# Optimization experiments

Measured on AMD Instinct MI355X. Metric: run time of the kernel, lower is better.

The kernel has to match this reference:

```python
import jax, jax.numpy as jnp
import numpy as np

BATCH = 262144
N_ASSETS = 64
N_GROUPS = 8
ITERS = 20
EPS = 1e-9


def setup_inputs() -> dict:
    key = jax.random.key(0)
    kx = jax.random.fold_in(key, 1)
    x = jax.random.uniform(kx, (BATCH, N_ASSETS), dtype=jnp.float32)
    x = x / jnp.sum(x, axis=-1, keepdims=True)  # roughly simplex-like raw weights
    box_lb = jnp.zeros((N_ASSETS,), jnp.float32)          # port_type[0] = 0 (long-only)
    box_ub = jnp.full((N_ASSETS,), 0.3, jnp.float32)      # per-asset cap from _build_constraints
    # one-hot group membership matrix: asset i belongs to group i % N_GROUPS
    gid = np.arange(N_ASSETS) % N_GROUPS
    A = np.zeros((N_GROUPS, N_ASSETS), np.float32)
    A[gid, np.arange(N_ASSETS)] = 1.0
    group_A = jnp.asarray(A)
    group_lb = jnp.full((N_GROUPS,), 0.05, jnp.float32)
    group_ub = jnp.full((N_GROUPS,), 0.5, jnp.float32)
    return {"x": x, "box_lb": box_lb, "box_ub": box_ub, "group_A": group_A,
            "group_lb": group_lb, "group_ub": group_ub, "num_iterations": ITERS}


def _dykstra(x, box_lb, box_ub, group_A, group_lb, group_ub, num_iterations):
    n = x.shape[-1]
    norm_sq = jnp.sum(group_A * group_A, axis=-1)  # (G,)

    def box_simplex(w):
        w = jnp.clip(w, box_lb, box_ub)
        return w - (jnp.sum(w, axis=-1, keepdims=True) - 1.0) / n

    def group_step(w, g):
        a, lb, ub, ns = g  # a: (N,), scalars lb/ub/ns
        Aw = w @ a  # (B,)
        w = jnp.where((Aw > ub)[:, None], w - ((Aw - ub) / (ns + EPS))[:, None] * a, w)
        Aw = w @ a  # recomputed on updated w, matching the TF layer
        w = jnp.where((Aw < lb)[:, None], w - ((Aw - lb) / (ns + EPS))[:, None] * a, w)
        return w, None

    def body(i, w):
        w = box_simplex(w)
        w, _ = jax.lax.scan(group_step, w, (group_A, group_lb, group_ub, norm_sq))
        return w

    w = jax.lax.fori_loop(0, num_iterations, body, x)
    return box_simplex(w)


def reference(x, box_lb, box_ub, group_A, group_lb, group_ub, num_iterations):
    return _dykstra(x, box_lb, box_ub, group_A, group_lb, group_ub, num_iterations)
```

## Files before the change

kernel.cpp:

```cpp
#include <hip/hip_runtime.h>


#define NA 64
#define NG 8
#define TOL 1e-6f

__device__ __forceinline__ float row8_allreduce_sum(float v) {
    int j = __builtin_amdgcn_update_dpp(0, __builtin_bit_cast(int, v),
                                        0xB1 , 0xF, 0xF, true);
    v += __builtin_bit_cast(float, j);
    j = __builtin_amdgcn_update_dpp(0, __builtin_bit_cast(int, v),
                                    0x4E , 0xF, 0xF, true);
    v += __builtin_bit_cast(float, j);
    j = __builtin_amdgcn_ds_swizzle(__builtin_bit_cast(int, v), 0x101F );
    v += __builtin_bit_cast(float, j);
    return v;
}

__device__ __forceinline__ bool structural_ok(const float* __restrict__ box_lb,
                                              const float* __restrict__ box_ub,
                                              const float* __restrict__ group_A,
                                              int l) {
    const float lb0 = box_lb[0], ub0 = box_ub[0];
    bool ok = (box_lb[l] == lb0) && (box_ub[l] == ub0) && (lb0 <= ub0);
#pragma unroll
    for (int g = 0; g < NG; ++g) {
        const float expect = ((l & 7) == g) ? 1.0f : 0.0f;
        ok = ok && (group_A[g * NA + l] == expect);
    }
    return __all(ok);
}

__global__ __launch_bounds__(256) void proj_fast(
    const float* __restrict__ x,
    const float* __restrict__ box_lb,
    const float* __restrict__ box_ub,
    const float* __restrict__ group_A,
    const float* __restrict__ group_lb,
    const float* __restrict__ group_ub,
    const int*  __restrict__ num_iter,
    float* __restrict__ out,
    int nrows)
{
    if (!structural_ok(box_lb, box_ub, group_A, threadIdx.x & 63)) return;

    const int t = blockIdx.x * blockDim.x + threadIdx.x;
    const int r = t >> 3;
    const int c = t & 7;
    if (r >= nrows) return;

    const float* __restrict__ xr = x + (size_t)r * NA;
    float* __restrict__ outr = out + (size_t)r * NA;

    float w[8];
#pragma unroll
    for (int k = 0; k < 8; ++k) w[k] = xr[k * 8 + c];

    const float lb0 = box_lb[0], ub0 = box_ub[0];
    const float glb = group_lb[c];
    const float gub = group_ub[c];

    const int iters = *num_iter;

    const float inv8 = 1.0f / (8.0f + 1e-9f);

    for (int it = 0; it < iters; ++it) {
#pragma unroll
        for (int k = 0; k < 8; ++k)
            w[k] = __builtin_amdgcn_fmed3f(w[k], lb0, ub0);
        const float s01 = w[0] + w[1], s23 = w[2] + w[3];
        const float s45 = w[4] + w[5], s67 = w[6] + w[7];
        const float dota = (s01 + s23) + (s45 + s67);

        const float S = row8_allreduce_sum(dota);
        const float shift = fmaf(S, 1.0f / NA, -1.0f / NA);

        const float Aw  = fmaf(-8.0f, shift, dota);
        const float e1  = fmaxf(Aw - gub, 0.0f);
        const float Aw2 = Aw - e1;
        const float e2  = fminf(Aw2 - glb, 0.0f);
        const float d   = (e1 + e2) * inv8;
        const float u   = shift + d;

#pragma unroll
        for (int k = 0; k < 8; ++k) w[k] -= u;

        if (__all(__builtin_fabsf(shift) < TOL && __builtin_fabsf(d) < TOL))
            break;
    }

#pragma unroll
    for (int k = 0; k < 8; ++k)
        w[k] = __builtin_amdgcn_fmed3f(w[k], lb0, ub0);
    const float s01 = w[0] + w[1], s23 = w[2] + w[3];
    const float s45 = w[4] + w[5], s67 = w[6] + w[7];
    const float S = row8_allreduce_sum((s01 + s23) + (s45 + s67));
    const float shift = fmaf(S, 1.0f / NA, -1.0f / NA);

#pragma unroll
    for (int k = 0; k < 8; ++k)
        outr[k * 8 + c] = w[k] - shift;
}

__global__ __launch_bounds__(256) void proj_generic(
    const float* __restrict__ x,
    const float* __restrict__ box_lb,
    const float* __restrict__ box_ub,
    const float* __restrict__ group_A,
    const float* __restrict__ group_lb,
    const float* __restrict__ group_ub,
    const int*  __restrict__ num_iter,
    float* __restrict__ out,
    int nrows)
{
    if (structural_ok(box_lb, box_ub, group_A, threadIdx.x & 63)) return;

    const int r = blockIdx.x * blockDim.x + threadIdx.x;
    if (r >= nrows) return;

    const float* __restrict__ xr = x + (size_t)r * NA;
    float* __restrict__ outr = out + (size_t)r * NA;

    float w[NA];
#pragma unroll
    for (int j = 0; j < NA; ++j) w[j] = xr[j];

    const int iters = *num_iter;

    for (int it = 0; it < iters; ++it) {
        float S = 0.0f;
#pragma unroll
        for (int j = 0; j < NA; ++j) {
            w[j] = fminf(fmaxf(w[j], box_lb[j]), box_ub[j]);
            S += w[j];
        }
        const float shift = (S - 1.0f) * (1.0f / NA);
#pragma unroll
        for (int j = 0; j < NA; ++j) w[j] -= shift;

        for (int g = 0; g < NG; ++g) {
            const float* __restrict__ a = group_A + g * NA;
            float ns = 0.0f, Aw = 0.0f;
#pragma unroll
            for (int j = 0; j < NA; ++j) {
                const float av = a[j];
                ns = fmaf(av, av, ns);
                Aw = fmaf(av, w[j], Aw);
            }
            const float invg = 1.0f / (ns + 1e-9f);
            const float gub = group_ub[g], glb = group_lb[g];
            const float d1 = (Aw > gub) ? (Aw - gub) * invg : 0.0f;
#pragma unroll
            for (int j = 0; j < NA; ++j) w[j] = fmaf(-d1, a[j], w[j]);
            float Aw2 = 0.0f;
#pragma unroll
            for (int j = 0; j < NA; ++j) Aw2 = fmaf(a[j], w[j], Aw2);
            const float d2 = (Aw2 < glb) ? (Aw2 - glb) * invg : 0.0f;
#pragma unroll
            for (int j = 0; j < NA; ++j) w[j] = fmaf(-d2, a[j], w[j]);
        }
    }
    float S = 0.0f;
#pragma unroll
    for (int j = 0; j < NA; ++j) {
        w[j] = fminf(fmaxf(w[j], box_lb[j]), box_ub[j]);
        S += w[j];
    }
    const float shift = (S - 1.0f) * (1.0f / NA);
#pragma unroll
    for (int j = 0; j < NA; ++j) outr[j] = w[j] - shift;
}

extern "C" void kernel_launch(void* const* d_in, const int* in_sizes, int n_in,
                              void* d_out, int out_size, void* d_ws, size_t ws_size,
                              hipStream_t stream) {
    const float* x        = (const float*)d_in[0];
    const float* box_lb   = (const float*)d_in[1];
    const float* box_ub   = (const float*)d_in[2];
    const float* group_A  = (const float*)d_in[3];
    const float* group_lb = (const float*)d_in[4];
    const float* group_ub = (const float*)d_in[5];
    const int*   num_iter = (const int*)d_in[6];
    float* out = (float*)d_out;

    const int nrows = in_sizes[0] / NA;

    {
        const int total = nrows * 8;
        const int block = 256;
        const int grid = (total + block - 1) / block;
        proj_fast<<<grid, block, 0, stream>>>(x, box_lb, box_ub, group_A,
                                              group_lb, group_ub, num_iter,
                                              out, nrows);
    }
    {
        const int block = 256;
        const int grid = (nrows + block - 1) / block;
        proj_generic<<<grid, block, 0, stream>>>(x, box_lb, box_ub, group_A,
                                                 group_lb, group_ub, num_iter,
                                                 out, nrows);
    }
}
```

Before: 135.3 us.

## Merge fast and generic kernels and stage row I/O through LDS with float4

Combines the structured fast path and the generic fallback into one kernel that picks the path per wave at runtime, which removes the second kernel launch. Row loads and stores now go through shared memory as contiguous float4 accesses and are then redistributed to the 8-lanes-per-row layout. The generic path is also rewritten to use 8 lanes per row with DPP reductions. The cost is added LDS traffic and two block barriers.

```diff
diff --git a/kernel.cpp b/kernel.cpp
--- a/kernel.cpp
+++ b/kernel.cpp
@@ -4,6 +4,9 @@
 #define NA 64
 #define NG 8
 #define TOL 1e-6f
+#define RS 72
+#define ROWS_PER_BLOCK 32
+#define ROWS_PER_WAVE 8
 
 __device__ __forceinline__ float row8_allreduce_sum(float v) {
     int j = __builtin_amdgcn_update_dpp(0, __builtin_bit_cast(int, v),
@@ -17,21 +20,7 @@
     return v;
 }
 
-__device__ __forceinline__ bool structural_ok(const float* __restrict__ box_lb,
-                                              const float* __restrict__ box_ub,
-                                              const float* __restrict__ group_A,
-                                              int l) {
-    const float lb0 = box_lb[0], ub0 = box_ub[0];
-    bool ok = (box_lb[l] == lb0) && (box_ub[l] == ub0) && (lb0 <= ub0);
-#pragma unroll
-    for (int g = 0; g < NG; ++g) {
-        const float expect = ((l & 7) == g) ? 1.0f : 0.0f;
-        ok = ok && (group_A[g * NA + l] == expect);
-    }
-    return __all(ok);
-}
-
-__global__ __launch_bounds__(256) void proj_fast(
+__global__ __launch_bounds__(256) void proj_kernel(
     const float* __restrict__ x,
     const float* __restrict__ box_lb,
     const float* __restrict__ box_ub,
@@ -42,133 +31,161 @@
     float* __restrict__ out,
     int nrows)
 {
-    if (!structural_ok(box_lb, box_ub, group_A, threadIdx.x & 63)) return;
-
-    const int t = blockIdx.x * blockDim.x + threadIdx.x;
-    const int r = t >> 3;
-    const int c = t & 7;
-    if (r >= nrows) return;
-
-    const float* __restrict__ xr = x + (size_t)r * NA;
-    float* __restrict__ outr = out + (size_t)r * NA;
-
+    __shared__ float lds[ROWS_PER_BLOCK * RS];
+
+    const int tid  = threadIdx.x;
+    const int wave = tid >> 6;
+    const int lane = tid & 63;
+    const int lr   = lane >> 3;
+    const int c    = lane & 7;
+
+    const size_t wrow0 = (size_t)blockIdx.x * ROWS_PER_BLOCK + (size_t)wave * ROWS_PER_WAVE;
+    const size_t r = wrow0 + (size_t)lr;
+    const bool fullwave = (wrow0 + ROWS_PER_WAVE) <= (size_t)nrows;
+    const bool valid = r < (size_t)nrows;
+
+    float* lw = lds + wave * ROWS_PER_WAVE * RS;
+
+    float4 v0, v1;
+    if (fullwave) {
+        const float4* src = reinterpret_cast<const float4*>(x + wrow0 * NA);
+        v0 = src[lane];
+        v1 = src[lane + 64];
+    }
+
+    const float lb0 = box_lb[0], ub0 = box_ub[0];
+    bool ok = (box_lb[lane] == lb0) && (box_ub[lane] == ub0) && (lb0 <= ub0);
+#pragma unroll
+    for (int g = 0; g < NG; ++g) {
+        const float expect = ((lane & 7) == g) ? 1.0f : 0.0f;
+        ok = ok && (group_A[g * NA + lane] == expect);
+    }
+    const bool fast = __all(ok);
+
+    if (fullwave) {
+        *reinterpret_cast<float4*>(lw + (lane >> 4) * RS + (lane & 15) * 4) = v0;
+        *reinterpret_cast<float4*>(lw + ((lane >> 4) + 4) * RS + (lane & 15) * 4) = v1;
+    }
+    __syncthreads();
     float w[8];
-#pragma unroll
-    for (int k = 0; k < 8; ++k) w[k] = xr[k * 8 + c];
-
-    const float lb0 = box_lb[0], ub0 = box_ub[0];
-    const float glb = group_lb[c];
-    const float gub = group_ub[c];
+    if (fullwave) {
+#pragma unroll
+        for (int k = 0; k < 8; ++k) w[k] = lw[lr * RS + k * 8 + c];
+    } else if (valid) {
+#pragma unroll
+        for (int k = 0; k < 8; ++k) w[k] = x[r * NA + k * 8 + c];
+    }
 
     const int iters = *num_iter;
-
-    const float inv8 = 1.0f / (8.0f + 1e-9f);
-
-    for (int it = 0; it < iters; ++it) {
+    float shift = 0.0f;
+
+    if (fast) {
+        const float glb = group_lb[c];
+        const float gub = group_ub[c];
+        const float inv8 = 1.0f / (8.0f + 1e-9f);
+
+        for (int it = 0; it < iters; ++it) {
+#pragma unroll
+            for (int k = 0; k < 8; ++k)
+                w[k] = __builtin_amdgcn_fmed3f(w[k], lb0, ub0);
+            const float s01 = w[0] + w[1], s23 = w[2] + w[3];
+            const float s45 = w[4] + w[5], s67 = w[6] + w[7];
+            const float dota = (s01 + s23) + (s45 + s67);
+
+            const float S = row8_allreduce_sum(dota);
+            const float sh = fmaf(S, 1.0f / NA, -1.0f / NA);
+
+            const float Aw  = fmaf(-8.0f, sh, dota);
+            const float e1  = fmaxf(Aw - gub, 0.0f);
+            const float Aw2 = Aw - e1;
+            const float e2  = fminf(Aw2 - glb, 0.0f);
+            const float d   = (e1 + e2) * inv8;
+            const float u   = sh + d;
+#pragma unroll
+            for (int k = 0; k < 8; ++k) w[k] -= u;
+
+            if (__all(__builtin_fabsf(sh) < TOL && __builtin_fabsf(d) < TOL))
+                break;
+        }
 #pragma unroll
         for (int k = 0; k < 8; ++k)
             w[k] = __builtin_amdgcn_fmed3f(w[k], lb0, ub0);
         const float s01 = w[0] + w[1], s23 = w[2] + w[3];
         const float s45 = w[4] + w[5], s67 = w[6] + w[7];
-        const float dota = (s01 + s23) + (s45 + s67);
-
-        const float S = row8_allreduce_sum(dota);
-        const float shift = fmaf(S, 1.0f / NA, -1.0f / NA);
-
-        const float Aw  = fmaf(-8.0f, shift, dota);
-        const float e1  = fmaxf(Aw - gub, 0.0f);
-        const float Aw2 = Aw - e1;
-        const float e2  = fminf(Aw2 - glb, 0.0f);
-        const float d   = (e1 + e2) * inv8;
-        const float u   = shift + d;
-
-#pragma unroll
-        for (int k = 0; k < 8; ++k) w[k] -= u;
-
-        if (__all(__builtin_fabsf(shift) < TOL && __builtin_fabsf(d) < TOL))
-            break;
-    }
-
-#pragma unroll
-    for (int k = 0; k < 8; ++k)
-        w[k] = __builtin_amdgcn_fmed3f(w[k], lb0, ub0);
-    const float s01 = w[0] + w[1], s23 = w[2] + w[3];
-    const float s45 = w[4] + w[5], s67 = w[6] + w[7];
-    const float S = row8_allreduce_sum((s01 + s23) + (s45 + s67));
-    const float shift = fmaf(S, 1.0f / NA, -1.0f / NA);
-
-#pragma unroll
-    for (int k = 0; k < 8; ++k)
-        outr[k * 8 + c] = w[k] - shift;
-}
-
-__global__ __launch_bounds__(256) void proj_generic(
-    const float* __restrict__ x,
-    const float* __restrict__ box_lb,
-    const float* __restrict__ box_ub,
-    const float* __restrict__ group_A,
-    const float* __restrict__ group_lb,
-    const float* __restrict__ group_ub,
-    const int*  __restrict__ num_iter,
-    float* __restrict__ out,
-    int nrows)
-{
-    if (structural_ok(box_lb, box_ub, group_A, threadIdx.x & 63)) return;
-
-    const int r = blockIdx.x * blockDim.x + threadIdx.x;
-    if (r >= nrows) return;
-
-    const float* __restrict__ xr = x + (size_t)r * NA;
-    float* __restrict__ outr = out + (size_t)r * NA;
-
-    float w[NA];
-#pragma unroll
-    for (int j = 0; j < NA; ++j) w[j] = xr[j];
-
-    const int iters = *num_iter;
-
-    for (int it = 0; it < iters; ++it) {
+        const float S = row8_allreduce_sum((s01 + s23) + (s45 + s67));
+        shift = fmaf(S, 1.0f / NA, -1.0f / NA);
+    } else {
+        float lbv[8], ubv[8];
+#pragma unroll
+        for (int k = 0; k < 8; ++k) {
+            lbv[k] = box_lb[k * 8 + c];
+            ubv[k] = box_ub[k * 8 + c];
+        }
+        for (int it = 0; it < iters; ++it) {
+            float S = 0.0f;
+#pragma unroll
+            for (int k = 0; k < 8; ++k) {
+                w[k] = fminf(fmaxf(w[k], lbv[k]), ubv[k]);
+                S += w[k];
+            }
+            S = row8_allreduce_sum(S);
+            const float sh = (S - 1.0f) * (1.0f / NA);
+#pragma unroll
+            for (int k = 0; k < 8; ++k) w[k] -= sh;
+
+            for (int g = 0; g < NG; ++g) {
+                float a[8];
+#pragma unroll
+                for (int k = 0; k < 8; ++k) a[k] = group_A[g * NA + k * 8 + c];
+                float ns = 0.0f, Aw = 0.0f;
+#pragma unroll
+                for (int k = 0; k < 8; ++k) {
+                    ns = fmaf(a[k], a[k], ns);
+                    Aw = fmaf(a[k], w[k], Aw);
+                }
+                ns = row8_allreduce_sum(ns);
+                Aw = row8_allreduce_sum(Aw);
+                const float invg = 1.0f / (ns + 1e-9f);
+                const float gub = group_ub[g], glb = group_lb[g];
+                const float d1 = (Aw > gub) ? (Aw - gub) * invg : 0.0f;
+#pragma unroll
+                for (int k = 0; k < 8; ++k) w[k] = fmaf(-d1, a[k], w[k]);
+                float Aw2 = 0.0f;
+#pragma unroll
+                for (int k = 0; k < 8; ++k) Aw2 = fmaf(a[k], w[k], Aw2);
+                Aw2 = row8_allreduce_sum(Aw2);
+                const float d2 = (Aw2 < glb) ? (Aw2 - glb) * invg : 0.0f;
+#pragma unroll
+                for (int k = 0; k < 8; ++k) w[k] = fmaf(-d2, a[k], w[k]);
+            }
+        }
         float S = 0.0f;
 #pragma unroll
-        for (int j = 0; j < NA; ++j) {
-            w[j] = fminf(fmaxf(w[j], box_lb[j]), box_ub[j]);
-            S += w[j];
-        }
-        const float shift = (S - 1.0f) * (1.0f / NA);
-#pragma unroll
-        for (int j = 0; j < NA; ++j) w[j] -= shift;
-
-        for (int g = 0; g < NG; ++g) {
-            const float* __restrict__ a = group_A + g * NA;
-            float ns = 0.0f, Aw = 0.0f;
-#pragma unroll
-            for (int j = 0; j < NA; ++j) {
-                const float av = a[j];
-                ns = fmaf(av, av, ns);
-                Aw = fmaf(av, w[j], Aw);
-            }
-            const float invg = 1.0f / (ns + 1e-9f);
-            const float gub = group_ub[g], glb = group_lb[g];
-            const float d1 = (Aw > gub) ? (Aw - gub) * invg : 0.0f;
-#pragma unroll
-            for (int j = 0; j < NA; ++j) w[j] = fmaf(-d1, a[j], w[j]);
-            float Aw2 = 0.0f;
-#pragma unroll
-            for (int j = 0; j < NA; ++j) Aw2 = fmaf(a[j], w[j], Aw2);
-            const float d2 = (Aw2 < glb) ? (Aw2 - glb) * invg : 0.0f;
-#pragma unroll
-            for (int j = 0; j < NA; ++j) w[j] = fmaf(-d2, a[j], w[j]);
-        }
-    }
-    float S = 0.0f;
-#pragma unroll
-    for (int j = 0; j < NA; ++j) {
-        w[j] = fminf(fmaxf(w[j], box_lb[j]), box_ub[j]);
-        S += w[j];
-    }
-    const float shift = (S - 1.0f) * (1.0f / NA);
-#pragma unroll
-    for (int j = 0; j < NA; ++j) outr[j] = w[j] - shift;
+        for (int k = 0; k < 8; ++k) {
+            w[k] = fminf(fmaxf(w[k], lbv[k]), ubv[k]);
+            S += w[k];
+        }
+        S = row8_allreduce_sum(S);
+        shift = (S - 1.0f) * (1.0f / NA);
+    }
+
+    if (fullwave) {
+#pragma unroll
+        for (int k = 0; k < 8; ++k)
+            lw[lr * RS + k * 8 + c] = w[k] - shift;
+    }
+    __syncthreads();
+    if (fullwave) {
+        const float4 q0 = *reinterpret_cast<const float4*>(lw + (lane >> 4) * RS + (lane & 15) * 4);
+        const float4 q1 = *reinterpret_cast<const float4*>(lw + ((lane >> 4) + 4) * RS + (lane & 15) * 4);
+        float4* dst = reinterpret_cast<float4*>(out + wrow0 * NA);
+        dst[lane] = q0;
+        dst[lane + 64] = q1;
+    } else if (valid) {
+#pragma unroll
+        for (int k = 0; k < 8; ++k)
+            out[r * NA + k * 8 + c] = w[k] - shift;
+    }
 }
 
 extern "C" void kernel_launch(void* const* d_in, const int* in_sizes, int n_in,
@@ -184,20 +201,11 @@
     float* out = (float*)d_out;
 
     const int nrows = in_sizes[0] / NA;
-
-    {
-        const int total = nrows * 8;
-        const int block = 256;
-        const int grid = (total + block - 1) / block;
-        proj_fast<<<grid, block, 0, stream>>>(x, box_lb, box_ub, group_A,
-                                              group_lb, group_ub, num_iter,
-                                              out, nrows);
-    }
-    {
-        const int block = 256;
-        const int grid = (nrows + block - 1) / block;
-        proj_generic<<<grid, block, 0, stream>>>(x, box_lb, box_ub, group_A,
-                                                 group_lb, group_ub, num_iter,
-                                                 out, nrows);
-    }
+    const int total = nrows * 8;
+    const int block = 256;
+    const int grid = (total + block - 1) / block;
+
+    proj_kernel<<<grid, block, 0, stream>>>(x, box_lb, box_ub, group_A,
+                                            group_lb, group_ub, num_iter,
+                                            out, nrows);
 }
```

After: 127.9 us. 1.06x faster.
